# Performance work log

Measured on AMD Instinct MI355X. Metric: run time of the kernel, lower is better.

The kernel has to match this reference:

```python
import jax, jax.numpy as jnp
import numpy as np

N_TEST = 16384
NUM_CLASSES = 1000
TEMPERATURE = 2.0


def setup_inputs() -> dict:
    key = jax.random.key(0)
    ks = jax.random.split(key, 6)
    mk = lambda k: jax.random.normal(k, (N_TEST, NUM_CLASSES), dtype=jnp.float32)
    return {
        "outputs1": mk(ks[0]),
        "outputs2": mk(ks[1]),
        "outputs3": mk(ks[2]),
        "outputs4": mk(ks[3]),
        "mimic": mk(ks[4]),
        "targets": jax.random.randint(ks[5], (N_TEST,), 0, NUM_CLASSES, dtype=jnp.int64),
        "n_test": N_TEST,
    }


def _margin(o, targets):
    # top-2 reduction replaces the full descending sort (same top-2 values)
    top2, _ = jax.lax.top_k(o, 2)                                   # [n, 2]
    tgt_val = jnp.take_along_axis(o, targets[:, None], axis=1)[:, 0]  # [n]
    # margin = (max - second_max) only when target is the argmax value, else 0
    return jnp.where(top2[:, 0] == tgt_val, top2[:, 0] - top2[:, 1], jnp.zeros((), o.dtype))


def reference(outputs1, outputs2, outputs3, outputs4, mimic, targets, n_test):
    outs = (outputs1, outputs2, outputs3, outputs4, mimic)
    preds = jnp.stack([_margin(o, targets) for o in outs], axis=1)  # [n, 5]
    out_threshold = jax.nn.softmax(preds / TEMPERATURE, axis=1)
    max_preds = jnp.max(jnp.stack((outputs1, outputs2, outputs3, outputs4), axis=0))
    return max_preds, out_threshold
```

## Files before the change

### kernel.cpp

```cpp
#include <hip/hip_runtime.h>
#include <math.h>

#define NCLS  1000
#define NROWS 16384
#define INV_TEMP 0.5f
#define NEG_INF (-INFINITY)

__device__ __forceinline__ void merge2(float& a1, float& a2, float b1, float b2) {
    const float mn = fminf(a1, b1);
    a1 = fmaxf(a1, b1);
    a2 = fmaxf(mn, fmaxf(a2, b2));
}

__device__ __forceinline__ void top2_wave(const float4& v0, const float4& v1,
                                          const float4& v2, const float4& v3,
                                          float& m1, float& m2)
{
    float t1[4], t2[4];
    const float4 vv[4] = {v0, v1, v2, v3};
    #pragma unroll
    for (int i = 0; i < 4; ++i) {
        const float hi1 = fmaxf(vv[i].x, vv[i].y), lo1 = fminf(vv[i].x, vv[i].y);
        const float hi2 = fmaxf(vv[i].z, vv[i].w), lo2 = fminf(vv[i].z, vv[i].w);
        t1[i] = fmaxf(hi1, hi2);
        t2[i] = fmaxf(fminf(hi1, hi2), fmaxf(lo1, lo2));
    }
    merge2(t1[0], t2[0], t1[1], t2[1]);
    merge2(t1[2], t2[2], t1[3], t2[3]);
    merge2(t1[0], t2[0], t1[2], t2[2]);
    m1 = t1[0]; m2 = t2[0];
    #pragma unroll
    for (int off = 32; off >= 1; off >>= 1) {
        const float q1 = __shfl_xor(m1, off, 64);
        const float q2 = __shfl_xor(m2, off, 64);
        merge2(m1, m2, q1, q2);
    }
}

__device__ __forceinline__ float extract_tv(const float4& v0, const float4& v1,
                                            const float4& v2, const float4& v3,
                                            int tgt)
{
    const int q = tgt >> 2, comp = tgt & 3, chunk = q >> 6, src = q & 63;
    const float4 sel = (chunk == 0) ? v0 : (chunk == 1) ? v1
                     : (chunk == 2) ? v2 : v3;
    const float c = (comp == 0) ? sel.x : (comp == 1) ? sel.y
                  : (comp == 2) ? sel.z : sel.w;
    return __shfl(c, src, 64);
}

__global__ __launch_bounds__(256) void fused_margin_softmax(
    const float* __restrict__ o1, const float* __restrict__ o2,
    const float* __restrict__ o3, const float* __restrict__ o4,
    const float* __restrict__ mim, const int* __restrict__ targets,
    float* __restrict__ out, float* __restrict__ wavemax)
{
    const int lane = threadIdx.x & 63;
    const int row  = blockIdx.x * 4 + (threadIdx.x >> 6);
    const int i3   = (lane < 58) ? (192 + lane) : 249;

    const float4* pa = (const float4*)(o1  + (size_t)row * NCLS);
    const float4* pb = (const float4*)(o2  + (size_t)row * NCLS);
    const float4* pc = (const float4*)(o3  + (size_t)row * NCLS);
    const float4* pd = (const float4*)(o4  + (size_t)row * NCLS);
    const float4* pe = (const float4*)(mim + (size_t)row * NCLS);

    float4 a0 = pa[lane], a1 = pa[64 + lane], a2 = pa[128 + lane], a3 = pa[i3];
    float4 b0 = pb[lane], b1 = pb[64 + lane], b2 = pb[128 + lane], b3 = pb[i3];
    float4 c0 = pc[lane], c1 = pc[64 + lane], c2 = pc[128 + lane], c3 = pc[i3];
    float4 d0 = pd[lane], d1 = pd[64 + lane], d2 = pd[128 + lane], d3 = pd[i3];
    float4 e0 = pe[lane], e1 = pe[64 + lane], e2 = pe[128 + lane], e3 = pe[i3];
    const int tgt = targets[row];

    if (lane >= 58) {
        const float4 n4 = make_float4(NEG_INF, NEG_INF, NEG_INF, NEG_INF);
        a3 = n4; b3 = n4; c3 = n4; d3 = n4; e3 = n4;
    }

    float m1, m2, tv, rowmax;
    float g0, g1, g2, g3, g4;

    tv = extract_tv(a0, a1, a2, a3, tgt);
    top2_wave(a0, a1, a2, a3, m1, m2);
    g0 = (m1 == tv) ? (m1 - m2) : 0.0f;
    rowmax = m1;

    tv = extract_tv(b0, b1, b2, b3, tgt);
    top2_wave(b0, b1, b2, b3, m1, m2);
    g1 = (m1 == tv) ? (m1 - m2) : 0.0f;
    rowmax = fmaxf(rowmax, m1);

    tv = extract_tv(c0, c1, c2, c3, tgt);
    top2_wave(c0, c1, c2, c3, m1, m2);
    g2 = (m1 == tv) ? (m1 - m2) : 0.0f;
    rowmax = fmaxf(rowmax, m1);

    tv = extract_tv(d0, d1, d2, d3, tgt);
    top2_wave(d0, d1, d2, d3, m1, m2);
    g3 = (m1 == tv) ? (m1 - m2) : 0.0f;
    rowmax = fmaxf(rowmax, m1);

    tv = extract_tv(e0, e1, e2, e3, tgt);
    top2_wave(e0, e1, e2, e3, m1, m2);
    g4 = (m1 == tv) ? (m1 - m2) : 0.0f;

    const float q0 = g0 * INV_TEMP, q1 = g1 * INV_TEMP, q2 = g2 * INV_TEMP,
                q3 = g3 * INV_TEMP, q4 = g4 * INV_TEMP;
    const float pm = fmaxf(fmaxf(fmaxf(q0, q1), fmaxf(q2, q3)), q4);
    const float x0 = expf(q0 - pm), x1 = expf(q1 - pm), x2 = expf(q2 - pm),
                x3 = expf(q3 - pm), x4 = expf(q4 - pm);
    const float inv = 1.0f / (x0 + x1 + x2 + x3 + x4);

    if (lane < 5) {
        const float r = (lane == 0) ? x0 : (lane == 1) ? x1 : (lane == 2) ? x2
                      : (lane == 3) ? x3 : x4;
        out[1 + (size_t)row * 5 + lane] = r * inv;
    }
    if (lane == 5) wavemax[row] = rowmax;
}

__global__ __launch_bounds__(1024) void final_max_kernel(
    const float* __restrict__ wavemax, float* __restrict__ out)
{
    const float4* w4 = (const float4*)wavemax;
    float m = NEG_INF;
    #pragma unroll
    for (int i = 0; i < (NROWS / 4) / 1024; ++i) {
        const float4 v = w4[threadIdx.x + i * 1024];
        m = fmaxf(fmaxf(fmaxf(m, v.x), v.y), fmaxf(v.z, v.w));
    }
    #pragma unroll
    for (int off = 32; off >= 1; off >>= 1)
        m = fmaxf(m, __shfl_xor(m, off, 64));
    __shared__ float s[16];
    const int lane = threadIdx.x & 63, wid = threadIdx.x >> 6;
    if (lane == 0) s[wid] = m;
    __syncthreads();
    if (threadIdx.x == 0) {
        float mm = s[0];
        #pragma unroll
        for (int i = 1; i < 16; ++i) mm = fmaxf(mm, s[i]);
        out[0] = mm;
    }
}

extern "C" void kernel_launch(void* const* d_in, const int* in_sizes, int n_in,
                              void* d_out, int out_size, void* d_ws, size_t ws_size,
                              hipStream_t stream) {
    const float* o1  = (const float*)d_in[0];
    const float* o2  = (const float*)d_in[1];
    const float* o3  = (const float*)d_in[2];
    const float* o4  = (const float*)d_in[3];
    const float* mim = (const float*)d_in[4];
    const int*   tgt = (const int*)d_in[5];

    float* out = (float*)d_out;
    float* wavemax = (float*)d_ws;

    fused_margin_softmax<<<NROWS / 4, 256, 0, stream>>>(o1, o2, o3, o4, mim, tgt,
                                                        out, wavemax);
    final_max_kernel<<<1, 1024, 0, stream>>>(wavemax, out);
}
```

Before: 292.2 us.

## Switch to block-per-row persistent kernel with register prefetch of next row

Instead of one wave per row with four float4 loads per matrix, each 256-thread block now handles a row with one float4 per thread and strides over 8 rows. It prefetches the next row into registers while reducing the current one. The top-2 reduction now crosses waves through LDS with a __syncthreads per row, and thread 0 does the final merge and softmax serially. The aim is to overlap loads with compute and shrink the partial-max buffer, at the cost of extra block-level synchronisation and a serial tail on one thread per row.

Measured after the change: 307.4 us. 1.05x slower.

```diff
diff --git a/kernel.cpp b/kernel.cpp
--- a/kernel.cpp
+++ b/kernel.cpp
@@ -1,8 +1,11 @@
 #include <hip/hip_runtime.h>
 #include <math.h>
 
-#define NCLS  1000
-#define NROWS 16384
+#define NCLS   1000
+#define NV4    250
+#define NROWS  16384
+#define NBLOCKS 2048
+#define ROWS_PER_BLOCK (NROWS / NBLOCKS)
 #define INV_TEMP 0.5f
 #define NEG_INF (-INFINITY)
 
@@ -12,122 +15,122 @@
     a2 = fmaxf(mn, fmaxf(a2, b2));
 }
 
-__device__ __forceinline__ void top2_wave(const float4& v0, const float4& v1,
-                                          const float4& v2, const float4& v3,
-                                          float& m1, float& m2)
-{
-    float t1[4], t2[4];
-    const float4 vv[4] = {v0, v1, v2, v3};
-    #pragma unroll
-    for (int i = 0; i < 4; ++i) {
-        const float hi1 = fmaxf(vv[i].x, vv[i].y), lo1 = fminf(vv[i].x, vv[i].y);
-        const float hi2 = fmaxf(vv[i].z, vv[i].w), lo2 = fminf(vv[i].z, vv[i].w);
-        t1[i] = fmaxf(hi1, hi2);
-        t2[i] = fmaxf(fminf(hi1, hi2), fmaxf(lo1, lo2));
-    }
-    merge2(t1[0], t2[0], t1[1], t2[1]);
-    merge2(t1[2], t2[2], t1[3], t2[3]);
-    merge2(t1[0], t2[0], t1[2], t2[2]);
-    m1 = t1[0]; m2 = t2[0];
-    #pragma unroll
-    for (int off = 32; off >= 1; off >>= 1) {
-        const float q1 = __shfl_xor(m1, off, 64);
-        const float q2 = __shfl_xor(m2, off, 64);
-        merge2(m1, m2, q1, q2);
-    }
+__device__ __forceinline__ void top2_of4(const float4 v, float& t1, float& t2) {
+    const float hi1 = fmaxf(v.x, v.y), lo1 = fminf(v.x, v.y);
+    const float hi2 = fmaxf(v.z, v.w), lo2 = fminf(v.z, v.w);
+    t1 = fmaxf(hi1, hi2);
+    t2 = fmaxf(fminf(hi1, hi2), fmaxf(lo1, lo2));
 }
 
-__device__ __forceinline__ float extract_tv(const float4& v0, const float4& v1,
-                                            const float4& v2, const float4& v3,
-                                            int tgt)
-{
-    const int q = tgt >> 2, comp = tgt & 3, chunk = q >> 6, src = q & 63;
-    const float4 sel = (chunk == 0) ? v0 : (chunk == 1) ? v1
-                     : (chunk == 2) ? v2 : v3;
-    const float c = (comp == 0) ? sel.x : (comp == 1) ? sel.y
-                  : (comp == 2) ? sel.z : sel.w;
-    return __shfl(c, src, 64);
-}
-
-__global__ __launch_bounds__(256) void fused_margin_softmax(
+__global__ __launch_bounds__(256) void fused_persistent(
     const float* __restrict__ o1, const float* __restrict__ o2,
     const float* __restrict__ o3, const float* __restrict__ o4,
     const float* __restrict__ mim, const int* __restrict__ targets,
-    float* __restrict__ out, float* __restrict__ wavemax)
+    float* __restrict__ out, float* __restrict__ blockmax)
 {
-    const int lane = threadIdx.x & 63;
-    const int row  = blockIdx.x * 4 + (threadIdx.x >> 6);
-    const int i3   = (lane < 58) ? (192 + lane) : 249;
+    const int tid  = threadIdx.x;
+    const int lane = tid & 63;
+    const int wid  = tid >> 6;
+    const bool act = (tid < NV4);
+    const int  li  = act ? tid : (NV4 - 1);
 
-    const float4* pa = (const float4*)(o1  + (size_t)row * NCLS);
-    const float4* pb = (const float4*)(o2  + (size_t)row * NCLS);
-    const float4* pc = (const float4*)(o3  + (size_t)row * NCLS);
-    const float4* pd = (const float4*)(o4  + (size_t)row * NCLS);
-    const float4* pe = (const float4*)(mim + (size_t)row * NCLS);
+    const float4* mats[5] = {
+        (const float4*)o1, (const float4*)o2, (const float4*)o3,
+        (const float4*)o4, (const float4*)mim };
 
-    float4 a0 = pa[lane], a1 = pa[64 + lane], a2 = pa[128 + lane], a3 = pa[i3];
-    float4 b0 = pb[lane], b1 = pb[64 + lane], b2 = pb[128 + lane], b3 = pb[i3];
-    float4 c0 = pc[lane], c1 = pc[64 + lane], c2 = pc[128 + lane], c3 = pc[i3];
-    float4 d0 = pd[lane], d1 = pd[64 + lane], d2 = pd[128 + lane], d3 = pd[i3];
-    float4 e0 = pe[lane], e1 = pe[64 + lane], e2 = pe[128 + lane], e3 = pe[i3];
-    const int tgt = targets[row];
+    __shared__ float lds[2][4][5][2];
+    __shared__ float ltv[2][5];
 
-    if (lane >= 58) {
-        const float4 n4 = make_float4(NEG_INF, NEG_INF, NEG_INF, NEG_INF);
-        a3 = n4; b3 = n4; c3 = n4; d3 = n4; e3 = n4;
+    int r = blockIdx.x;
+    float4 nxt[5];
+    #pragma unroll
+    for (int m = 0; m < 5; ++m) nxt[m] = mats[m][(size_t)r * NV4 + li];
+    int tnxt = targets[r];
+
+    float bmax = NEG_INF;
+
+    #pragma unroll
+    for (int it = 0; it < ROWS_PER_BLOCK; ++it) {
+        float4 cur[5];
+        #pragma unroll
+        for (int m = 0; m < 5; ++m) cur[m] = nxt[m];
+        const int tcur = tnxt;
+        const int rn = r + NBLOCKS;
+        if (it + 1 < ROWS_PER_BLOCK) {
+            #pragma unroll
+            for (int m = 0; m < 5; ++m) nxt[m] = mats[m][(size_t)rn * NV4 + li];
+            tnxt = targets[rn];
+        }
+
+        const int buf = it & 1;
+
+        if (act && tid == (tcur >> 2)) {
+            const int comp = tcur & 3;
+            #pragma unroll
+            for (int m = 0; m < 5; ++m) {
+                const float4 v = cur[m];
+                ltv[buf][m] = (comp == 0) ? v.x : (comp == 1) ? v.y
+                            : (comp == 2) ? v.z : v.w;
+            }
+        }
+
+        #pragma unroll
+        for (int m = 0; m < 5; ++m) {
+            float t1, t2;
+            if (act) top2_of4(cur[m], t1, t2);
+            else     { t1 = NEG_INF; t2 = NEG_INF; }
+            #pragma unroll
+            for (int off = 32; off >= 1; off >>= 1) {
+                const float q1 = __shfl_xor(t1, off, 64);
+                const float q2 = __shfl_xor(t2, off, 64);
+                merge2(t1, t2, q1, q2);
+            }
+            if (lane == 0) { lds[buf][wid][m][0] = t1; lds[buf][wid][m][1] = t2; }
+        }
+
+        __syncthreads();
+
+        if (tid == 0) {
+            float g[5];
+            float rmax = NEG_INF;
+            #pragma unroll
+            for (int m = 0; m < 5; ++m) {
+                float m1 = lds[buf][0][m][0], m2 = lds[buf][0][m][1];
+                merge2(m1, m2, lds[buf][1][m][0], lds[buf][1][m][1]);
+                merge2(m1, m2, lds[buf][2][m][0], lds[buf][2][m][1]);
+                merge2(m1, m2, lds[buf][3][m][0], lds[buf][3][m][1]);
+                g[m] = (m1 == ltv[buf][m]) ? (m1 - m2) : 0.0f;
+                if (m < 4) rmax = fmaxf(rmax, m1);
+            }
+            bmax = fmaxf(bmax, rmax);
+
+            const float q0 = g[0] * INV_TEMP, q1 = g[1] * INV_TEMP,
+                        q2 = g[2] * INV_TEMP, q3 = g[3] * INV_TEMP,
+                        q4 = g[4] * INV_TEMP;
+            const float pm = fmaxf(fmaxf(fmaxf(q0, q1), fmaxf(q2, q3)), q4);
+            const float x0 = expf(q0 - pm), x1 = expf(q1 - pm),
+                        x2 = expf(q2 - pm), x3 = expf(q3 - pm),
+                        x4 = expf(q4 - pm);
+            const float inv = 1.0f / (x0 + x1 + x2 + x3 + x4);
+            float* b = out + 1 + (size_t)r * 5;
+            b[0] = x0 * inv; b[1] = x1 * inv; b[2] = x2 * inv;
+            b[3] = x3 * inv; b[4] = x4 * inv;
+        }
+
+        r = rn;
     }
 
-    float m1, m2, tv, rowmax;
-    float g0, g1, g2, g3, g4;
-
-    tv = extract_tv(a0, a1, a2, a3, tgt);
-    top2_wave(a0, a1, a2, a3, m1, m2);
-    g0 = (m1 == tv) ? (m1 - m2) : 0.0f;
-    rowmax = m1;
-
-    tv = extract_tv(b0, b1, b2, b3, tgt);
-    top2_wave(b0, b1, b2, b3, m1, m2);
-    g1 = (m1 == tv) ? (m1 - m2) : 0.0f;
-    rowmax = fmaxf(rowmax, m1);
-
-    tv = extract_tv(c0, c1, c2, c3, tgt);
-    top2_wave(c0, c1, c2, c3, m1, m2);
-    g2 = (m1 == tv) ? (m1 - m2) : 0.0f;
-    rowmax = fmaxf(rowmax, m1);
-
-    tv = extract_tv(d0, d1, d2, d3, tgt);
-    top2_wave(d0, d1, d2, d3, m1, m2);
-    g3 = (m1 == tv) ? (m1 - m2) : 0.0f;
-    rowmax = fmaxf(rowmax, m1);
-
-    tv = extract_tv(e0, e1, e2, e3, tgt);
-    top2_wave(e0, e1, e2, e3, m1, m2);
-    g4 = (m1 == tv) ? (m1 - m2) : 0.0f;
-
-    const float q0 = g0 * INV_TEMP, q1 = g1 * INV_TEMP, q2 = g2 * INV_TEMP,
-                q3 = g3 * INV_TEMP, q4 = g4 * INV_TEMP;
-    const float pm = fmaxf(fmaxf(fmaxf(q0, q1), fmaxf(q2, q3)), q4);
-    const float x0 = expf(q0 - pm), x1 = expf(q1 - pm), x2 = expf(q2 - pm),
-                x3 = expf(q3 - pm), x4 = expf(q4 - pm);
-    const float inv = 1.0f / (x0 + x1 + x2 + x3 + x4);
-
-    if (lane < 5) {
-        const float r = (lane == 0) ? x0 : (lane == 1) ? x1 : (lane == 2) ? x2
-                      : (lane == 3) ? x3 : x4;
-        out[1 + (size_t)row * 5 + lane] = r * inv;
-    }
-    if (lane == 5) wavemax[row] = rowmax;
+    if (tid == 0) blockmax[blockIdx.x] = bmax;
 }
 
 __global__ __launch_bounds__(1024) void final_max_kernel(
-    const float* __restrict__ wavemax, float* __restrict__ out)
+    const float* __restrict__ blockmax, float* __restrict__ out)
 {
-    const float4* w4 = (const float4*)wavemax;
+    const float4* w4 = (const float4*)blockmax;
     float m = NEG_INF;
-    #pragma unroll
-    for (int i = 0; i < (NROWS / 4) / 1024; ++i) {
-        const float4 v = w4[threadIdx.x + i * 1024];
-        m = fmaxf(fmaxf(fmaxf(m, v.x), v.y), fmaxf(v.z, v.w));
+    if (threadIdx.x < NBLOCKS / 4) {
+        const float4 v = w4[threadIdx.x];
+        m = fmaxf(fmaxf(v.x, v.y), fmaxf(v.z, v.w));
     }
     #pragma unroll
     for (int off = 32; off >= 1; off >>= 1)
@@ -155,9 +158,9 @@
     const int*   tgt = (const int*)d_in[5];
 
     float* out = (float*)d_out;
-    float* wavemax = (float*)d_ws;
+    float* blockmax = (float*)d_ws;
 
-    fused_margin_softmax<<<NROWS / 4, 256, 0, stream>>>(o1, o2, o3, o4, mim, tgt,
-                                                        out, wavemax);
-    final_max_kernel<<<1, 1024, 0, stream>>>(wavemax, out);
+    fused_persistent<<<NBLOCKS, 256, 0, stream>>>(o1, o2, o3, o4, mim, tgt,
+                                                  out, blockmax);
+    final_max_kernel<<<1, 1024, 0, stream>>>(blockmax, out);
 }
```
